# Kernel tuning notes

Measured on AMD Instinct MI355X. Metric: run time of the kernel, lower is better.

The kernel has to match this reference:

```python
import jax, jax.numpy as jnp
import numpy as np

N_NODES = 100000
D_FEAT = 128
UNITS = 128
N_EDGES = 600000


def setup_inputs() -> dict:
    key = jax.random.key(0)
    k1, k2, k3, k4, k5 = jax.random.split(key, 5)
    X = jax.random.normal(k1, (N_NODES, D_FEAT), dtype=jnp.float32)
    ref_a = jax.random.randint(k2, (N_EDGES,), 0, N_NODES, dtype=jnp.int32)
    ref_b = jax.random.randint(k3, (N_EDGES,), 0, N_NODES, dtype=jnp.int32)
    # Glorot-ish scaled dense weights
    W_hidden = jax.random.normal(k4, (D_FEAT, UNITS), dtype=jnp.float32) * (1.0 / np.sqrt(D_FEAT))
    W_out = jax.random.normal(k5, (UNITS, UNITS), dtype=jnp.float32) * (1.0 / np.sqrt(UNITS))
    b_hidden = jnp.zeros((UNITS,), dtype=jnp.float32)
    b_out = jnp.zeros((UNITS,), dtype=jnp.float32)
    return dict(X=X, ref_a=ref_a, ref_b=ref_b, W_hidden=W_hidden,
                b_hidden=b_hidden, W_out=W_out, b_out=b_out)


def wl1_convolution(X, ref_a, ref_b):
    # WL1 neighborhood aggregation over undirected edges (ref_a, ref_b):
    # each node keeps its own features plus the sum of its neighbors'.
    n = X.shape[0]
    agg_a = jax.ops.segment_sum(X[ref_b], ref_a, num_segments=n)  # [N, D]
    agg_b = jax.ops.segment_sum(X[ref_a], ref_b, num_segments=n)  # [N, D]
    return X + agg_a + agg_b


def reference(X, ref_a, ref_b, W_hidden, b_hidden, W_out, b_out):
    X_agg = wl1_convolution(X, ref_a, ref_b)                 # [N, D]
    X_hid = jax.nn.relu(X_agg @ W_hidden + b_hidden)          # [N, U] (inner_activation=relu)
    X_out = X_hid @ W_out + b_out                             # [N, U] (activation=linear)
    return X_out
```

## Files before the change

### kernel.cpp

```cpp
#include <hip/hip_runtime.h>

#define CAP 64
#define BCAP 4096
#define RADIX_UNITS 4096

typedef short bf16x8 __attribute__((ext_vector_type(8)));
typedef float f32x4 __attribute__((ext_vector_type(4)));
typedef unsigned short u16;
typedef unsigned int u32;

__device__ __forceinline__ u16 f32_to_bf16(float f) {
  u32 b = __float_as_uint(f);
  b += 0x7fffu + ((b >> 16) & 1u);
  return (u16)(b >> 16);
}

__global__ __launch_bounds__(256) void front_kernel(
    const float* __restrict__ X, u16* __restrict__ Xb, int n8,
    const int* __restrict__ ra, const int* __restrict__ rb,
    int* __restrict__ gOff, int2* __restrict__ binned, int nedges, int nunits,
    int nbins, int nradix) {
  if ((int)blockIdx.x >= nradix) {
    int i = ((int)blockIdx.x - nradix) * 256 + threadIdx.x;
    if (i >= n8) return;
    float4 a = ((const float4*)X)[2 * i];
    float4 b = ((const float4*)X)[2 * i + 1];
    int4 o;
    o.x = (int)((u32)f32_to_bf16(a.x) | ((u32)f32_to_bf16(a.y) << 16));
    o.y = (int)((u32)f32_to_bf16(a.z) | ((u32)f32_to_bf16(a.w) << 16));
    o.z = (int)((u32)f32_to_bf16(b.x) | ((u32)f32_to_bf16(b.y) << 16));
    o.w = (int)((u32)f32_to_bf16(b.z) | ((u32)f32_to_bf16(b.w) << 16));
    ((int4*)Xb)[i] = o;
    return;
  }
  __shared__ int lh[512];
  const int tid = threadIdx.x;
  for (int b = tid; b < nbins; b += 256) lh[b] = 0;
  __syncthreads();
  const int u0 = (int)blockIdx.x * RADIX_UNITS;

  for (int k = 0; k < RADIX_UNITS / 256; ++k) {
    int u = u0 + k * 256 + tid;
    if (u < nunits) {
      long long apk = ((const long long*)ra)[u];
      long long bpk = ((const long long*)rb)[u];
      int a0 = (int)apk, a1 = (int)(apk >> 32);
      int b0 = (int)bpk, b1 = (int)(bpk >> 32);
      bool has1 = (2 * u + 1) < nedges;
      atomicAdd(&lh[a0 >> 8], 1);
      atomicAdd(&lh[b0 >> 8], 1);
      if (has1) {
        atomicAdd(&lh[a1 >> 8], 1);
        atomicAdd(&lh[b1 >> 8], 1);
      }
    }
  }
  __syncthreads();
  for (int b = tid; b < nbins; b += 256) {
    int c = lh[b];
    lh[b] = (c > 0) ? atomicAdd(&gOff[b], c) : 0;
  }
  __syncthreads();
  for (int k = 0; k < RADIX_UNITS / 256; ++k) {
    int u = u0 + k * 256 + tid;
    if (u < nunits) {
      long long apk = ((const long long*)ra)[u];
      long long bpk = ((const long long*)rb)[u];
      int a0 = (int)apk, a1 = (int)(apk >> 32);
      int b0 = (int)bpk, b1 = (int)(bpk >> 32);
      bool has1 = (2 * u + 1) < nedges;
      int d[4], s[4];
      d[0] = a0; s[0] = b0;
      d[1] = b0; s[1] = a0;
      d[2] = has1 ? a1 : -1; s[2] = b1;
      d[3] = has1 ? b1 : -1; s[3] = a1;
#pragma unroll
      for (int i = 0; i < 4; ++i) {
        if (d[i] >= 0) {
          int b = d[i] >> 8;
          int slot = atomicAdd(&lh[b], 1);
          if (slot < BCAP) binned[(size_t)b * BCAP + slot] = make_int2(d[i], s[i]);
        }
      }
    }
  }
}

__global__ __launch_bounds__(256) void bin_build_kernel(
    const int2* __restrict__ binned, const int* __restrict__ gOff,
    int* __restrict__ cnt, int* __restrict__ adj, int nnodes) {
  __shared__ int lc[256];
  const int bin = blockIdx.x;
  lc[threadIdx.x] = 0;
  __syncthreads();
  int count = gOff[bin];
  if (count > BCAP) count = BCAP;
  const int2* src = binned + (size_t)bin * BCAP;
  for (int i = threadIdx.x; i < count; i += 256) {
    int2 e = src[i];
    int p = atomicAdd(&lc[e.x & 255], 1);
    if (p < CAP) adj[(size_t)e.x * CAP + p] = e.y;
  }
  __syncthreads();
  int node = bin * 256 + threadIdx.x;
  if (node < nnodes) cnt[node] = lc[threadIdx.x];
}

__global__ void gather_agg_kernel(const u16* __restrict__ Xb,
                                  const int* __restrict__ cnt,
                                  int* __restrict__ adj, int nnodes) {
  int gid = blockIdx.x * blockDim.x + threadIdx.x;
  int wid = gid >> 6;
  int l = gid & 63;
  int half = l >> 5;
  int hl = l & 31;
  int node = wid * 2 + half;
  if (node >= nnodes) return;
  const uint2* Xv = (const uint2*)Xb;
  const int* lst = adj + (size_t)node * CAP;
  int n = cnt[node];
  if (n > CAP) n = CAP;
  int idx0 = lst[hl];
  int idx1 = (n > 32) ? lst[hl + 32] : 0;
  uint2 ps = Xv[(size_t)node * 32 + hl];
  float a0 = __uint_as_float(ps.x << 16);
  float a1 = __uint_as_float(ps.x & 0xffff0000u);
  float a2 = __uint_as_float(ps.y << 16);
  float a3 = __uint_as_float(ps.y & 0xffff0000u);
  const int base = half << 5;
  for (int k = 0; k < n; k += 8) {
    uint2 pv[8];
#pragma unroll
    for (int t = 0; t < 8; ++t) {
      int pos = k + t;
      int sel = (pos < 32) ? idx0 : idx1;
      int nb = __shfl(sel, base + (pos & 31));
      pv[t] = (pos < n) ? Xv[(size_t)nb * 32 + hl] : make_uint2(0u, 0u);
    }
#pragma unroll
    for (int t = 0; t < 8; ++t) {
      a0 += __uint_as_float(pv[t].x << 16);
      a1 += __uint_as_float(pv[t].x & 0xffff0000u);
      a2 += __uint_as_float(pv[t].y << 16);
      a3 += __uint_as_float(pv[t].y & 0xffff0000u);
    }
  }
  u32 w0 = (u32)f32_to_bf16(a0) | ((u32)f32_to_bf16(a1) << 16);
  u32 w1 = (u32)f32_to_bf16(a2) | ((u32)f32_to_bf16(a3) << 16);
  ((uint2*)adj)[(size_t)node * 32 + hl] = make_uint2(w0, w1);
}

__global__ void convert_w_kernel(const float* __restrict__ Wh,
                                 const float* __restrict__ Wo,
                                 u16* __restrict__ WhT,
                                 u16* __restrict__ WoT) {
  int idx = blockIdx.x * 256 + threadIdx.x;
  const float* src = (idx < 16384) ? Wh : Wo;
  u16* dst = (idx < 16384) ? WhT : WoT;
  int i = idx & 16383;
  int k = i >> 7, n = i & 127;
  dst[n * 128 + k] = f32_to_bf16(src[k * 128 + n]);
}

__global__ __launch_bounds__(256) void mlp_mfma_kernel(
    const u16* __restrict__ Xagg,
    const u16* __restrict__ WhT,
    const u16* __restrict__ WoT,
    const float* __restrict__ bh,
    const float* __restrict__ bo,
    float* __restrict__ out, int nnodes) {
  __shared__ u16 smem[2 * 128 * 128];
  u16* sA = smem;
  u16* sW = smem + 16384;

  const int tid = threadIdx.x;
  const int w = tid >> 6;
  const int l = tid & 63;
  const int l15 = l & 15;
  const int l4 = l >> 4;
  const int r0 = blockIdx.x * 128;

#pragma unroll
  for (int t = 0; t < 8; ++t) {
    int id = tid + t * 256;
    int r = id >> 4, u = id & 15;
    int gr = r0 + r;
    if (gr >= nnodes) gr = nnodes - 1;
    *(int4*)&sA[r * 128 + ((u ^ (r & 15)) * 8)] =
        *(const int4*)&Xagg[(size_t)gr * 128 + u * 8];
    *(int4*)&sW[r * 128 + ((u ^ (r & 15)) * 8)] =
        *(const int4*)&WhT[r * 128 + u * 8];
  }

  float bhv[8], bov[8];
#pragma unroll
  for (int j = 0; j < 8; ++j) {
    bhv[j] = bh[j * 16 + l15];
    bov[j] = bo[j * 16 + l15];
  }
  __syncthreads();

  const int m0 = w * 32 + l15;
  const int m1 = w * 32 + 16 + l15;

  f32x4 acc[2][8];
#pragma unroll
  for (int i = 0; i < 2; ++i)
#pragma unroll
    for (int j = 0; j < 8; ++j) acc[i][j] = (f32x4){0.f, 0.f, 0.f, 0.f};

#pragma unroll
  for (int c = 0; c < 4; ++c) {
    int pu = ((c * 4 + l4) ^ l15) * 8;
    bf16x8 a0 = *(bf16x8*)&sA[m0 * 128 + pu];
    bf16x8 a1 = *(bf16x8*)&sA[m1 * 128 + pu];
#pragma unroll
    for (int j = 0; j < 8; ++j) {
      bf16x8 bfr = *(bf16x8*)&sW[(j * 16 + l15) * 128 + pu];
      acc[0][j] = __builtin_amdgcn_mfma_f32_16x16x32_bf16(a0, bfr, acc[0][j], 0, 0, 0);
      acc[1][j] = __builtin_amdgcn_mfma_f32_16x16x32_bf16(a1, bfr, acc[1][j], 0, 0, 0);
    }
  }

  __syncthreads();

#pragma unroll
  for (int t = 0; t < 8; ++t) {
    int id = tid + t * 256;
    int r = id >> 4, u = id & 15;
    *(int4*)&sW[r * 128 + ((u ^ (r & 15)) * 8)] =
        *(const int4*)&WoT[r * 128 + u * 8];
  }

#pragma unroll
  for (int i = 0; i < 2; ++i)
#pragma unroll
    for (int j = 0; j < 8; ++j)
#pragma unroll
      for (int r = 0; r < 4; ++r) {
        int m = w * 32 + i * 16 + l4 * 4 + r;
        float v = fmaxf(acc[i][j][r] + bhv[j], 0.f);
        int k = j * 16 + l15;
        sA[m * 128 + (((k >> 3) ^ (m & 15)) * 8) + (k & 7)] = f32_to_bf16(v);
      }
  __syncthreads();

#pragma unroll
  for (int i = 0; i < 2; ++i)
#pragma unroll
    for (int j = 0; j < 8; ++j) acc[i][j] = (f32x4){0.f, 0.f, 0.f, 0.f};

#pragma unroll
  for (int c = 0; c < 4; ++c) {
    int pu = ((c * 4 + l4) ^ l15) * 8;
    bf16x8 a0 = *(bf16x8*)&sA[m0 * 128 + pu];
    bf16x8 a1 = *(bf16x8*)&sA[m1 * 128 + pu];
#pragma unroll
    for (int j = 0; j < 8; ++j) {
      bf16x8 bfr = *(bf16x8*)&sW[(j * 16 + l15) * 128 + pu];
      acc[0][j] = __builtin_amdgcn_mfma_f32_16x16x32_bf16(a0, bfr, acc[0][j], 0, 0, 0);
      acc[1][j] = __builtin_amdgcn_mfma_f32_16x16x32_bf16(a1, bfr, acc[1][j], 0, 0, 0);
    }
  }

  __syncthreads();

  float* sOut = (float*)smem;
#pragma unroll
  for (int i = 0; i < 2; ++i)
#pragma unroll
    for (int j = 0; j < 8; ++j)
#pragma unroll
      for (int r = 0; r < 4; ++r) {
        int m = w * 32 + i * 16 + l4 * 4 + r;
        sOut[m * 128 + j * 16 + l15] = acc[i][j][r] + bov[j];
      }
  __syncthreads();
#pragma unroll
  for (int t = 0; t < 16; ++t) {
    int id = tid + t * 256;
    int r = id >> 5, u4 = id & 31;
    int gr = r0 + r;
    if (gr < nnodes)
      ((float4*)out)[(size_t)gr * 32 + u4] = ((const float4*)sOut)[id];
  }
}

extern "C" void kernel_launch(void* const* d_in, const int* in_sizes, int n_in,
                              void* d_out, int out_size, void* d_ws,
                              size_t ws_size, hipStream_t stream) {
  const float* X = (const float*)d_in[0];
  const int* ra = (const int*)d_in[1];
  const int* rb = (const int*)d_in[2];
  const float* Wh = (const float*)d_in[3];
  const float* bh = (const float*)d_in[4];
  const float* Wo = (const float*)d_in[5];
  const float* bo = (const float*)d_in[6];
  float* out = (float*)d_out;

  int nnodes = in_sizes[0] / 128;
  int nedges = in_sizes[1];
  int nunits = (nedges + 1) / 2;
  int nbins = (nnodes + 255) >> 8;
  int nradix = (nunits + RADIX_UNITS - 1) / RADIX_UNITS;

  int* cnt = (int*)d_ws;
  int* adj = cnt + nnodes;
  u16* WhT = (u16*)d_ws;
  u16* WoT = WhT + 16384;
  u16* Xb = (u16*)d_out;
  int2* binned = (int2*)((char*)d_out + (size_t)nnodes * 256);
  int* gOff = (int*)((char*)binned + (size_t)nbins * BCAP * sizeof(int2));

  int n8 = nnodes * 16;
  int nconv = (n8 + 255) / 256;
  hipMemsetAsync(gOff, 0, (size_t)nbins * 4, stream);
  front_kernel<<<nradix + nconv, 256, 0, stream>>>(
      X, Xb, n8, ra, rb, gOff, binned, nedges, nunits, nbins, nradix);
  bin_build_kernel<<<nbins, 256, 0, stream>>>(binned, gOff, cnt, adj, nnodes);
  int nwaves = (nnodes + 1) / 2;
  gather_agg_kernel<<<(nwaves * 64 + 255) / 256, 256, 0, stream>>>(Xb, cnt,
                                                                   adj, nnodes);
  convert_w_kernel<<<128, 256, 0, stream>>>(Wh, Wo, WhT, WoT);
  mlp_mfma_kernel<<<(nnodes + 127) / 128, 256, 0, stream>>>(
      (const u16*)adj, WhT, WoT, bh, bo, out, nnodes);
}
```

Baseline: 211.6 us.

## Fuse adjacency bin build into gather aggregation using shared-memory neighbor lists

Merges the bin-build and gather-aggregate kernels into one. Each pair of blocks handles a 256-node bin: every block reads the whole binned edge list, keeps only edges for its 128 nodes, and builds their neighbor lists in LDS. It then gathers neighbor features straight from those lists, so the global adjacency array, the count array and one kernel launch go away. In exchange, each bin's edges are read twice, the blocks use a large LDS footprint (32KB lists), and the gather phase runs at lower parallelism per block (16 sequential node iterations per wave pair).

```diff
diff --git a/kernel.cpp b/kernel.cpp
--- a/kernel.cpp
+++ b/kernel.cpp
@@ -86,68 +86,67 @@
   }
 }
 
-__global__ __launch_bounds__(256) void bin_build_kernel(
-    const int2* __restrict__ binned, const int* __restrict__ gOff,
-    int* __restrict__ cnt, int* __restrict__ adj, int nnodes) {
-  __shared__ int lc[256];
-  const int bin = blockIdx.x;
-  lc[threadIdx.x] = 0;
+__global__ __launch_bounds__(256) void gather_bin_kernel(
+    const u16* __restrict__ Xb, const int2* __restrict__ binned,
+    const int* __restrict__ gOff, int* __restrict__ xagg, int nnodes) {
+  __shared__ int lists[128 * CAP];
+  __shared__ int lc[128];
+  const int tid = threadIdx.x;
+  const int bin = blockIdx.x >> 1;
+  const int sub = blockIdx.x & 1;
+  if (tid < 128) lc[tid] = 0;
   __syncthreads();
   int count = gOff[bin];
   if (count > BCAP) count = BCAP;
   const int2* src = binned + (size_t)bin * BCAP;
-  for (int i = threadIdx.x; i < count; i += 256) {
+  const int lo = sub << 7;
+  for (int i = tid; i < count; i += 256) {
     int2 e = src[i];
-    int p = atomicAdd(&lc[e.x & 255], 1);
-    if (p < CAP) adj[(size_t)e.x * CAP + p] = e.y;
-  }
-  __syncthreads();
-  int node = bin * 256 + threadIdx.x;
-  if (node < nnodes) cnt[node] = lc[threadIdx.x];
-}
-
-__global__ void gather_agg_kernel(const u16* __restrict__ Xb,
-                                  const int* __restrict__ cnt,
-                                  int* __restrict__ adj, int nnodes) {
-  int gid = blockIdx.x * blockDim.x + threadIdx.x;
-  int wid = gid >> 6;
-  int l = gid & 63;
-  int half = l >> 5;
-  int hl = l & 31;
-  int node = wid * 2 + half;
-  if (node >= nnodes) return;
+    int loc = (e.x & 255) - lo;
+    if ((unsigned)loc < 128u) {
+      int p = atomicAdd(&lc[loc], 1);
+      if (p < CAP) lists[loc * CAP + p] = e.y;
+    }
+  }
+  __syncthreads();
+
+  const int w = tid >> 6;
+  const int l = tid & 63;
+  const int half = l >> 5;
+  const int hl = l & 31;
   const uint2* Xv = (const uint2*)Xb;
-  const int* lst = adj + (size_t)node * CAP;
-  int n = cnt[node];
-  if (n > CAP) n = CAP;
-  int idx0 = lst[hl];
-  int idx1 = (n > 32) ? lst[hl + 32] : 0;
-  uint2 ps = Xv[(size_t)node * 32 + hl];
-  float a0 = __uint_as_float(ps.x << 16);
-  float a1 = __uint_as_float(ps.x & 0xffff0000u);
-  float a2 = __uint_as_float(ps.y << 16);
-  float a3 = __uint_as_float(ps.y & 0xffff0000u);
-  const int base = half << 5;
-  for (int k = 0; k < n; k += 8) {
-    uint2 pv[8];
-#pragma unroll
-    for (int t = 0; t < 8; ++t) {
-      int pos = k + t;
-      int sel = (pos < 32) ? idx0 : idx1;
-      int nb = __shfl(sel, base + (pos & 31));
-      pv[t] = (pos < n) ? Xv[(size_t)nb * 32 + hl] : make_uint2(0u, 0u);
-    }
-#pragma unroll
-    for (int t = 0; t < 8; ++t) {
-      a0 += __uint_as_float(pv[t].x << 16);
-      a1 += __uint_as_float(pv[t].x & 0xffff0000u);
-      a2 += __uint_as_float(pv[t].y << 16);
-      a3 += __uint_as_float(pv[t].y & 0xffff0000u);
-    }
-  }
-  u32 w0 = (u32)f32_to_bf16(a0) | ((u32)f32_to_bf16(a1) << 16);
-  u32 w1 = (u32)f32_to_bf16(a2) | ((u32)f32_to_bf16(a3) << 16);
-  ((uint2*)adj)[(size_t)node * 32 + hl] = make_uint2(w0, w1);
+  for (int p = 0; p < 16; ++p) {
+    int lr = p * 8 + w * 2 + half;
+    int v = (bin << 8) + lo + lr;
+    if (v >= nnodes) continue;
+    int n = lc[lr];
+    if (n > CAP) n = CAP;
+    const int* myl = &lists[lr * CAP];
+    uint2 ps = Xv[(size_t)v * 32 + hl];
+    float a0 = __uint_as_float(ps.x << 16);
+    float a1 = __uint_as_float(ps.x & 0xffff0000u);
+    float a2 = __uint_as_float(ps.y << 16);
+    float a3 = __uint_as_float(ps.y & 0xffff0000u);
+    for (int k = 0; k < n; k += 8) {
+      uint2 pv[8];
+#pragma unroll
+      for (int t = 0; t < 8; ++t) {
+        int pos = k + t;
+        int nb = myl[pos];
+        pv[t] = (pos < n) ? Xv[(size_t)nb * 32 + hl] : make_uint2(0u, 0u);
+      }
+#pragma unroll
+      for (int t = 0; t < 8; ++t) {
+        a0 += __uint_as_float(pv[t].x << 16);
+        a1 += __uint_as_float(pv[t].x & 0xffff0000u);
+        a2 += __uint_as_float(pv[t].y << 16);
+        a3 += __uint_as_float(pv[t].y & 0xffff0000u);
+      }
+    }
+    u32 w0 = (u32)f32_to_bf16(a0) | ((u32)f32_to_bf16(a1) << 16);
+    u32 w1 = (u32)f32_to_bf16(a2) | ((u32)f32_to_bf16(a3) << 16);
+    ((uint2*)xagg)[(size_t)v * 32 + hl] = make_uint2(w0, w1);
+  }
 }
 
 __global__ void convert_w_kernel(const float* __restrict__ Wh,
@@ -304,24 +303,22 @@
   int nbins = (nnodes + 255) >> 8;
   int nradix = (nunits + RADIX_UNITS - 1) / RADIX_UNITS;
 
-  int* cnt = (int*)d_ws;
-  int* adj = cnt + nnodes;
   u16* WhT = (u16*)d_ws;
   u16* WoT = WhT + 16384;
+  int* xagg = (int*)d_ws + nnodes;
+
   u16* Xb = (u16*)d_out;
   int2* binned = (int2*)((char*)d_out + (size_t)nnodes * 256);
   int* gOff = (int*)((char*)binned + (size_t)nbins * BCAP * sizeof(int2));
 
   int n8 = nnodes * 16;
   int nconv = (n8 + 255) / 256;
-  hipMemsetAsync(gOff, 0, (size_t)nbins * 4, stream);
+  (void)hipMemsetAsync(gOff, 0, (size_t)nbins * 4, stream);
   front_kernel<<<nradix + nconv, 256, 0, stream>>>(
       X, Xb, n8, ra, rb, gOff, binned, nedges, nunits, nbins, nradix);
-  bin_build_kernel<<<nbins, 256, 0, stream>>>(binned, gOff, cnt, adj, nnodes);
-  int nwaves = (nnodes + 1) / 2;
-  gather_agg_kernel<<<(nwaves * 64 + 255) / 256, 256, 0, stream>>>(Xb, cnt,
-                                                                   adj, nnodes);
+  gather_bin_kernel<<<nbins * 2, 256, 0, stream>>>(Xb, binned, gOff, xagg,
+                                                   nnodes);
   convert_w_kernel<<<128, 256, 0, stream>>>(Wh, Wo, WhT, WoT);
   mlp_mfma_kernel<<<(nnodes + 127) / 128, 256, 0, stream>>>(
-      (const u16*)adj, WhT, WoT, bh, bo, out, nnodes);
-}
+      (const u16*)xagg, WhT, WoT, bh, bo, out, nnodes);
+}
```

Measured after the change: 207.4 us. About the same (-2.0%).
